# Kernel tuning notes

Measured on AMD Instinct MI355X. Metric: run time of the kernel, lower is better.

The kernel has to match this reference:

```python
import jax, jax.numpy as jnp
import numpy as np

NUM_HEADS = 12


def setup_inputs() -> dict:
    key = jax.random.key(0)
    ks = jax.random.split(key, 5)
    B, N, D = 8, 1024, 768
    x = jax.random.normal(ks[0], (B, N, D), dtype=jnp.float32)
    w_qkv = jax.random.normal(ks[1], (D, 3 * D), dtype=jnp.float32) * (D ** -0.5)
    b_qkv = jax.random.normal(ks[2], (3 * D,), dtype=jnp.float32) * 0.02
    w_proj = jax.random.normal(ks[3], (D, D), dtype=jnp.float32) * (D ** -0.5)
    b_proj = jax.random.normal(ks[4], (D,), dtype=jnp.float32) * 0.02
    return {"x": x, "w_qkv": w_qkv, "b_qkv": b_qkv, "w_proj": w_proj, "b_proj": b_proj}


def reference(x, w_qkv, b_qkv, w_proj, b_proj):
    B, N, D = x.shape
    H = NUM_HEADS
    hd = D // H
    scale = hd ** -0.5
    qkv = x @ w_qkv + b_qkv                      # [B, N, 3D]
    qkv = qkv.reshape(B, N, 3, H, hd)
    q, k, v = jnp.moveaxis(qkv, 2, 0)            # each [B, N, H, hd]
    # scores: [B, H, N, N]
    scores = jnp.einsum("bqhd,bkhd->bhqk", q, k) * scale
    attn = jax.nn.softmax(scores, axis=-1)
    a = jnp.einsum("bhqk,bkhd->bqhd", attn, v)   # [B, N, H, hd]
    a = a.reshape(B, N, D)
    return a @ w_proj + b_proj
```

## Files before the change

kernel.cpp:

```cpp
#include <hip/hip_runtime.h>

#define B_ 8
#define N_ 1024
#define D_ 768
#define H_ 12
#define HD 64
#define M_ (B_*N_)

typedef short short8 __attribute__((ext_vector_type(8)));
typedef float f32x4 __attribute__((ext_vector_type(4)));
typedef float f32x16 __attribute__((ext_vector_type(16)));
typedef int int4v __attribute__((ext_vector_type(4)));

__device__ __forceinline__ unsigned short f2bf(float f) {
    union { float f; unsigned int u; } c; c.f = f;
    unsigned int u = c.u;
    unsigned int r = (u + 0x7fffu + ((u >> 16) & 1u)) >> 16;
    return (unsigned short)r;
}

__device__ __forceinline__ float exp2_hw(float x) {
    float r;
    asm("v_exp_f32 %0, %1" : "=v"(r) : "v"(x));
    return r;
}

__device__ __forceinline__ unsigned int cvtpk_bf16(float a, float b) {
    unsigned int r;
    asm("v_cvt_pk_bf16_f32 %0, %1, %2" : "=v"(r) : "v"(a), "v"(b));
    return r;
}

#define PLSWAP(a, b) asm volatile("v_permlane32_swap_b32 %0, %1" : "+&v"(a), "+&v"(b))

__device__ __forceinline__ short8 pack4(unsigned int a, unsigned int b,
                                        unsigned int c, unsigned int d) {
    union { int4v i; short8 s; } u;
    u.i = (int4v){(int)a, (int)b, (int)c, (int)d};
    return u.s;
}

__device__ __forceinline__ void gload16(const void* g, void* l) {
    __builtin_amdgcn_global_load_lds(
        (const __attribute__((address_space(1))) unsigned int*)g,
        (__attribute__((address_space(3))) unsigned int*)l, 16, 0, 0);
}


__global__ void cast_x_kernel(const float* __restrict__ in,
                              unsigned short* __restrict__ out, int n4) {
    int i = blockIdx.x * blockDim.x + threadIdx.x;
    if (i >= n4) return;
    float4 v = reinterpret_cast<const float4*>(in)[i];
    ushort4 o;
    o.x = f2bf(v.x); o.y = f2bf(v.y); o.z = f2bf(v.z); o.w = f2bf(v.w);
    reinterpret_cast<ushort4*>(out)[i] = o;
}

__global__ void transpose_cast_kernel(const float* __restrict__ w,
                                      unsigned short* __restrict__ wT,
                                      int R, int C) {
    int i = blockIdx.x * blockDim.x + threadIdx.x;
    if (i >= R * C) return;
    int r = i / C, c = i - r * C;
    wT[c * R + r] = f2bf(w[i]);
}

__global__ __launch_bounds__(256) void transpose_v_kernel(
    const unsigned short* __restrict__ vin,
    unsigned short* __restrict__ vout)
{
    __shared__ unsigned short T[64][72];
    int bh = blockIdx.y;
    int n0 = blockIdx.x * 64;
    int t = threadIdx.x;
    int r = t >> 2;
    int c = (t & 3) * 16;
    const uint4* g = reinterpret_cast<const uint4*>(vin + ((size_t)bh * N_ + n0 + r) * HD + c);
    uint4 a = g[0], b2 = g[1];
    *reinterpret_cast<uint4*>(&T[r][c]) = a;
    *reinterpret_cast<uint4*>(&T[r][c + 8]) = b2;
    __syncthreads();
    int d = t >> 2;
    int nc = (t & 3) * 16;
    unsigned short tmp[16];
    #pragma unroll
    for (int j = 0; j < 16; j++) tmp[j] = T[nc + j][d];
    uint4* o = reinterpret_cast<uint4*>(vout + ((size_t)bh * HD + d) * N_ + n0 + nc);
    o[0] = *reinterpret_cast<const uint4*>(&tmp[0]);
    o[1] = *reinterpret_cast<const uint4*>(&tmp[8]);
}


template<int MODE>
__global__ __launch_bounds__(256) void gemm_kernel(
    const unsigned short* __restrict__ A,
    const unsigned short* __restrict__ Bt,
    const float* __restrict__ bias,
    float* __restrict__ outf,
    unsigned short* __restrict__ qo,
    unsigned short* __restrict__ ko,
    unsigned short* __restrict__ vo,
    int Ndim, int K)
{
    __shared__ unsigned short As[128 * 32];
    __shared__ unsigned short Bs[128 * 32];

    int tid = threadIdx.x;
    int lane = tid & 63, w = tid >> 6;
    int wr = w >> 1, wc = w & 1;
    int m0 = blockIdx.y * 128, n0 = blockIdx.x * 128;
    int lr = lane & 15, lk8 = (lane >> 4) * 8;

    int srow = tid >> 2;
    int selem = (tid & 3) * 8;
    const unsigned short* gA = A + (size_t)(m0 + srow) * K + selem;
    const unsigned short* gB = Bt + (size_t)(n0 + srow) * K + selem;
    unsigned short* lA = As + w * 512;
    unsigned short* lB = Bs + w * 512;

    f32x4 acc[4][4] = {};

    for (int k0 = 0; k0 < K; k0 += 32) {
        __syncthreads();
        gload16(gA + k0, lA);
        gload16(gA + (size_t)64 * K + k0, lA + 2048);
        gload16(gB + k0, lB);
        gload16(gB + (size_t)64 * K + k0, lB + 2048);
        __syncthreads();

        short8 af[4], bf[4];
        #pragma unroll
        for (int mi = 0; mi < 4; mi++)
            af[mi] = *reinterpret_cast<const short8*>(&As[(wr * 64 + mi * 16 + lr) * 32 + lk8]);
        #pragma unroll
        for (int ni = 0; ni < 4; ni++)
            bf[ni] = *reinterpret_cast<const short8*>(&Bs[(wc * 64 + ni * 16 + lr) * 32 + lk8]);
        #pragma unroll
        for (int mi = 0; mi < 4; mi++)
            #pragma unroll
            for (int ni = 0; ni < 4; ni++)
                acc[mi][ni] = __builtin_amdgcn_mfma_f32_16x16x32_bf16(af[mi], bf[ni], acc[mi][ni], 0, 0, 0);
    }

    int org = (lane >> 4) * 4;
    if (MODE == 1) {
        #pragma unroll
        for (int mi = 0; mi < 4; mi++) {
            #pragma unroll
            for (int ni = 0; ni < 4; ni++) {
                int col = n0 + wc * 64 + ni * 16 + lr;
                float bv = bias[col];
                #pragma unroll
                for (int r = 0; r < 4; r++) {
                    int row = m0 + wr * 64 + mi * 16 + org + r;
                    outf[(size_t)row * Ndim + col] = acc[mi][ni][r] + bv;
                }
            }
        }
    } else {
        int which = n0 / 768;
        unsigned short* dst = (which == 0) ? qo : (which == 1) ? ko : vo;
        float fold = (which == 0) ? 0.125f * 1.44269504088896f : 1.0f;
        #pragma unroll
        for (int mi = 0; mi < 4; mi++) {
            #pragma unroll
            for (int ni = 0; ni < 4; ni++) {
                int col = n0 + wc * 64 + ni * 16 + lr;
                int rem = col - which * 768;
                int h = rem >> 6, dd = rem & 63;
                float bv = bias[col];
                #pragma unroll
                for (int r = 0; r < 4; r++) {
                    int row = m0 + wr * 64 + mi * 16 + org + r;
                    int b = row >> 10, nn = row & 1023;
                    float o = (acc[mi][ni][r] + bv) * fold;
                    dst[(((size_t)(b * H_ + h) * N_ + nn) * HD) + dd] = f2bf(o);
                }
            }
        }
    }
}


__global__ __launch_bounds__(256) void attn_kernel(
    const unsigned short* __restrict__ qg,
    const unsigned short* __restrict__ kg,
    const unsigned short* __restrict__ vtg,
    unsigned short* __restrict__ aout)
{
    __shared__ alignas(16) unsigned short Ks[2][4096];
    __shared__ alignas(16) unsigned short Vs[2][4096];

    int tid = threadIdx.x;
    int lane = tid & 63, w = tid >> 6;

    int bid = blockIdx.x;
    int xcd = bid & 7;
    int chunk = bid >> 3;
    int bh = xcd * 12 + (chunk % 12);
    int qblk = chunk / 12;
    int b = bh / H_, h = bh - b * H_;
    int q0w = qblk * 128 + w * 32;
    int l31 = lane & 31;
    int hi = lane >> 5;
    int swz = l31 & 7;

    const unsigned short* qp = qg + ((size_t)bh * N_ + q0w + l31) * HD + hi * 8;
    short8 qf[4];
    #pragma unroll
    for (int ds = 0; ds < 4; ds++)
        qf[ds] = *reinterpret_cast<const short8*>(qp + ds * 16);

    const unsigned short* kbh = kg + (size_t)bh * N_ * HD;
    const unsigned short* vtbh = vtg + (size_t)bh * HD * N_;

    int sr0 = tid >> 3;
    int sj0 = (tid & 7) ^ (sr0 & 7);
    int sr1 = sr0 + 32;
    int sj1 = (tid & 7) ^ (sr1 & 7);

    float m_run = -INFINITY, l_run = 0.f;
    f32x16 o0 = {}, o1 = {};

#define STAGE(buf, kv0)                                                        \
    do {                                                                       \
        gload16(kbh + (size_t)((kv0) + sr0) * HD + sj0 * 8, &Ks[buf][w * 512]);\
        gload16(kbh + (size_t)((kv0) + sr1) * HD + sj1 * 8, &Ks[buf][2048 + w * 512]);\
        gload16(vtbh + (size_t)sr0 * N_ + (kv0) + sj0 * 8, &Vs[buf][w * 512]); \
        gload16(vtbh + (size_t)sr1 * N_ + (kv0) + sj1 * 8, &Vs[buf][2048 + w * 512]);\
    } while (0)

    STAGE(0, 0);
    asm volatile("s_waitcnt vmcnt(0)" ::: "memory");
    __builtin_amdgcn_s_barrier();
    __builtin_amdgcn_sched_barrier(0);

    int cur = 0;
    for (int t = 0; t < 16; ++t) {
        if (t < 15) STAGE(cur ^ 1, (t + 1) * 64);

        const unsigned short* Ksb = Ks[cur];
        const unsigned short* Vsb = Vs[cur];

        f32x16 s0 = {}, s1 = {};
        #pragma unroll
        for (int ds = 0; ds < 4; ds++) {
            int pc = (ds * 2 + hi) ^ swz;
            short8 kf0 = *reinterpret_cast<const short8*>(&Ksb[(l31) * 64 + pc * 8]);
            short8 kf1 = *reinterpret_cast<const short8*>(&Ksb[(32 + l31) * 64 + pc * 8]);
            s0 = __builtin_amdgcn_mfma_f32_32x32x16_bf16(kf0, qf[ds], s0, 0, 0, 0);
            s1 = __builtin_amdgcn_mfma_f32_32x32x16_bf16(kf1, qf[ds], s1, 0, 0, 0);
        }

        float mx = s0[0];
        #pragma unroll
        for (int r = 1; r < 16; r++) mx = fmaxf(mx, s0[r]);
        #pragma unroll
        for (int r = 0; r < 16; r++) mx = fmaxf(mx, s1[r]);
        mx = fmaxf(mx, __shfl_xor(mx, 32, 64));

        if (__any(mx > m_run + 8.f)) {
            float mn = fmaxf(m_run, mx);
            float al = exp2_hw(m_run - mn);
            m_run = mn;
            l_run *= al;
            o0 *= al;
            o1 *= al;
        }

        float psum = 0.f;
        #pragma unroll
        for (int r = 0; r < 16; r++) { float p = exp2_hw(s0[r] - m_run); psum += p; s0[r] = p; }
        #pragma unroll
        for (int r = 0; r < 16; r++) { float p = exp2_hw(s1[r] - m_run); psum += p; s1[r] = p; }

        l_run += psum + __shfl_xor(psum, 32, 64);

        unsigned int c0[8], c1[8];
        #pragma unroll
        for (int i = 0; i < 8; i++) c0[i] = cvtpk_bf16(s0[2 * i], s0[2 * i + 1]);
        #pragma unroll
        for (int i = 0; i < 8; i++) c1[i] = cvtpk_bf16(s1[2 * i], s1[2 * i + 1]);
        PLSWAP(c0[0], c0[2]); PLSWAP(c0[1], c0[3]);
        PLSWAP(c0[4], c0[6]); PLSWAP(c0[5], c0[7]);
        PLSWAP(c1[0], c1[2]); PLSWAP(c1[1], c1[3]);
        PLSWAP(c1[4], c1[6]); PLSWAP(c1[5], c1[7]);
        short8 pa0 = pack4(c0[0], c0[1], c0[2], c0[3]);
        short8 pa1 = pack4(c0[4], c0[5], c0[6], c0[7]);
        short8 pa2 = pack4(c1[0], c1[1], c1[2], c1[3]);
        short8 pa3 = pack4(c1[4], c1[5], c1[6], c1[7]);

        #pragma unroll
        for (int ks = 0; ks < 4; ks++) {
            int pc = (ks * 2 + hi) ^ swz;
            short8 vf0 = *reinterpret_cast<const short8*>(&Vsb[(l31) * 64 + pc * 8]);
            short8 vf1 = *reinterpret_cast<const short8*>(&Vsb[(32 + l31) * 64 + pc * 8]);
            short8 pa = (ks == 0) ? pa0 : (ks == 1) ? pa1 : (ks == 2) ? pa2 : pa3;
            o0 = __builtin_amdgcn_mfma_f32_32x32x16_bf16(vf0, pa, o0, 0, 0, 0);
            o1 = __builtin_amdgcn_mfma_f32_32x32x16_bf16(vf1, pa, o1, 0, 0, 0);
        }

        if (t < 15) {
            asm volatile("s_waitcnt vmcnt(0)" ::: "memory");
            __builtin_amdgcn_s_barrier();
            __builtin_amdgcn_sched_barrier(0);
            cur ^= 1;
        }
    }
#undef STAGE

    float linv = 1.0f / l_run;
    unsigned short* op = aout + ((size_t)(b * N_ + q0w + l31)) * D_ + h * HD;
    #pragma unroll
    for (int rg = 0; rg < 4; rg++) {
        int dbase = 8 * rg + 4 * hi;
        unsigned long long u0 = 0, u1 = 0;
        #pragma unroll
        for (int k = 0; k < 4; k++) {
            u0 |= (unsigned long long)f2bf(o0[rg * 4 + k] * linv) << (16 * k);
            u1 |= (unsigned long long)f2bf(o1[rg * 4 + k] * linv) << (16 * k);
        }
        *reinterpret_cast<unsigned long long*>(op + dbase) = u0;
        *reinterpret_cast<unsigned long long*>(op + 32 + dbase) = u1;
    }
}


extern "C" void kernel_launch(void* const* d_in, const int* in_sizes, int n_in,
                              void* d_out, int out_size, void* d_ws, size_t ws_size,
                              hipStream_t stream) {
    const float* x      = (const float*)d_in[0];
    const float* w_qkv  = (const float*)d_in[1];
    const float* b_qkv  = (const float*)d_in[2];
    const float* w_proj = (const float*)d_in[3];
    const float* b_proj = (const float*)d_in[4];
    float* out = (float*)d_out;

    char* ws = (char*)d_ws;
    unsigned short* xb     = (unsigned short*)(ws + 0);
    unsigned short* wqkvT  = (unsigned short*)(ws + 12582912);
    unsigned short* wprojT = (unsigned short*)(ws + 16121856);
    unsigned short* qb     = (unsigned short*)(ws + 17301504);
    unsigned short* kb     = (unsigned short*)(ws + 29884416);
    unsigned short* vb     = (unsigned short*)(ws + 42467328);
    unsigned short* vtb    = (unsigned short*)(ws + 55050240);
    unsigned short* aout   = xb;

    cast_x_kernel<<<6144, 256, 0, stream>>>(x, xb, 1572864);
    transpose_cast_kernel<<<6912, 256, 0, stream>>>(w_qkv, wqkvT, 768, 2304);
    transpose_cast_kernel<<<2304, 256, 0, stream>>>(w_proj, wprojT, 768, 768);

    gemm_kernel<0><<<dim3(18, 64), 256, 0, stream>>>(
        xb, wqkvT, b_qkv, nullptr, qb, kb, vb, 3 * D_, D_);

    transpose_v_kernel<<<dim3(16, 96), 256, 0, stream>>>(vb, vtb);

    attn_kernel<<<768, 256, 0, stream>>>(qb, kb, vtb, aout);

    gemm_kernel<1><<<dim3(6, 64), 256, 0, stream>>>(
        aout, wprojT, b_proj, out, nullptr, nullptr, nullptr, D_, D_);
}
```

Measured before the change: 148.3 us.

## Merge prep kernels, double-buffer GEMM, fuse V transpose into QKV epilogue

Merges the three cast/transpose kernels into one launch. Double-buffers the GEMM's LDS tiles so the next k-slice loads while the current one is multiplied, and remaps the 1D grid so consecutive blocks are spread across XCDs. V is written already transposed from the QKV GEMM epilogue, which removes the separate transpose kernel and its round trip through memory. Q/K outputs are staged through LDS so each thread writes 16-byte vectors instead of scattered 2-byte stores. This adds code complexity and uses more LDS per GEMM block, which may lower occupancy.

```diff
diff --git a/kernel.cpp b/kernel.cpp
--- a/kernel.cpp
+++ b/kernel.cpp
@@ -47,48 +47,28 @@
 }
 
 
-__global__ void cast_x_kernel(const float* __restrict__ in,
-                              unsigned short* __restrict__ out, int n4) {
-    int i = blockIdx.x * blockDim.x + threadIdx.x;
-    if (i >= n4) return;
-    float4 v = reinterpret_cast<const float4*>(in)[i];
-    ushort4 o;
-    o.x = f2bf(v.x); o.y = f2bf(v.y); o.z = f2bf(v.z); o.w = f2bf(v.w);
-    reinterpret_cast<ushort4*>(out)[i] = o;
-}
-
-__global__ void transpose_cast_kernel(const float* __restrict__ w,
-                                      unsigned short* __restrict__ wT,
-                                      int R, int C) {
-    int i = blockIdx.x * blockDim.x + threadIdx.x;
-    if (i >= R * C) return;
-    int r = i / C, c = i - r * C;
-    wT[c * R + r] = f2bf(w[i]);
-}
-
-__global__ __launch_bounds__(256) void transpose_v_kernel(
-    const unsigned short* __restrict__ vin,
-    unsigned short* __restrict__ vout)
+__global__ __launch_bounds__(256) void prep_kernel(
+    const float* __restrict__ x, const float* __restrict__ wqkv,
+    const float* __restrict__ wproj,
+    unsigned short* __restrict__ xb, unsigned short* __restrict__ wqkvT,
+    unsigned short* __restrict__ wprojT)
 {
-    __shared__ unsigned short T[64][72];
-    int bh = blockIdx.y;
-    int n0 = blockIdx.x * 64;
-    int t = threadIdx.x;
-    int r = t >> 2;
-    int c = (t & 3) * 16;
-    const uint4* g = reinterpret_cast<const uint4*>(vin + ((size_t)bh * N_ + n0 + r) * HD + c);
-    uint4 a = g[0], b2 = g[1];
-    *reinterpret_cast<uint4*>(&T[r][c]) = a;
-    *reinterpret_cast<uint4*>(&T[r][c + 8]) = b2;
-    __syncthreads();
-    int d = t >> 2;
-    int nc = (t & 3) * 16;
-    unsigned short tmp[16];
-    #pragma unroll
-    for (int j = 0; j < 16; j++) tmp[j] = T[nc + j][d];
-    uint4* o = reinterpret_cast<uint4*>(vout + ((size_t)bh * HD + d) * N_ + n0 + nc);
-    o[0] = *reinterpret_cast<const uint4*>(&tmp[0]);
-    o[1] = *reinterpret_cast<const uint4*>(&tmp[8]);
+    int bid = blockIdx.x, tid = threadIdx.x;
+    if (bid < 6144) {
+        int i = bid * 256 + tid;
+        float4 v = reinterpret_cast<const float4*>(x)[i];
+        ushort4 o;
+        o.x = f2bf(v.x); o.y = f2bf(v.y); o.z = f2bf(v.z); o.w = f2bf(v.w);
+        reinterpret_cast<ushort4*>(xb)[i] = o;
+    } else if (bid < 6144 + 6912) {
+        int i = (bid - 6144) * 256 + tid;
+        int r = i / 2304, c = i - r * 2304;
+        wqkvT[c * 768 + r] = f2bf(wqkv[i]);
+    } else {
+        int i = (bid - 13056) * 256 + tid;
+        int r = i / 768, c = i - r * 768;
+        wprojT[c * 768 + r] = f2bf(wproj[i]);
+    }
 }
 
 
@@ -103,47 +83,73 @@
     unsigned short* __restrict__ vo,
     int Ndim, int K)
 {
-    __shared__ unsigned short As[128 * 32];
-    __shared__ unsigned short Bs[128 * 32];
+    __shared__ alignas(16) unsigned short smem[16384];
+    unsigned short* As0 = smem;
+    unsigned short* Bs0 = smem + 8192;
 
     int tid = threadIdx.x;
     int lane = tid & 63, w = tid >> 6;
     int wr = w >> 1, wc = w & 1;
-    int m0 = blockIdx.y * 128, n0 = blockIdx.x * 128;
+
+    int nbx = Ndim >> 7;
+    int nwg = gridDim.x;
+    int cpx = nwg >> 3;
+    int sbid = (blockIdx.x & 7) * cpx + (blockIdx.x >> 3);
+    int bx = sbid % nbx, by = sbid / nbx;
+    int m0 = by * 128, n0 = bx * 128;
+
     int lr = lane & 15, lk8 = (lane >> 4) * 8;
+    int org = (lane >> 4) * 4;
 
     int srow = tid >> 2;
     int selem = (tid & 3) * 8;
     const unsigned short* gA = A + (size_t)(m0 + srow) * K + selem;
     const unsigned short* gB = Bt + (size_t)(n0 + srow) * K + selem;
-    unsigned short* lA = As + w * 512;
-    unsigned short* lB = Bs + w * 512;
 
     f32x4 acc[4][4] = {};
 
-    for (int k0 = 0; k0 < K; k0 += 32) {
-        __syncthreads();
-        gload16(gA + k0, lA);
-        gload16(gA + (size_t)64 * K + k0, lA + 2048);
-        gload16(gB + k0, lB);
-        gload16(gB + (size_t)64 * K + k0, lB + 2048);
-        __syncthreads();
-
+#define GSTAGE(buf, k0)                                                    \
+    do {                                                                   \
+        gload16(gA + (k0), As0 + (buf) * 4096 + w * 512);                  \
+        gload16(gA + (size_t)64 * K + (k0), As0 + (buf) * 4096 + 2048 + w * 512);\
+        gload16(gB + (k0), Bs0 + (buf) * 4096 + w * 512);                  \
+        gload16(gB + (size_t)64 * K + (k0), Bs0 + (buf) * 4096 + 2048 + w * 512);\
+    } while (0)
+
+    GSTAGE(0, 0);
+    asm volatile("s_waitcnt vmcnt(0)" ::: "memory");
+    __builtin_amdgcn_s_barrier();
+    __builtin_amdgcn_sched_barrier(0);
+
+    int KT = K >> 5;
+    int cur = 0;
+    for (int kt = 0; kt < KT; ++kt) {
+        if (kt + 1 < KT) GSTAGE(cur ^ 1, (kt + 1) * 32);
+
+        const unsigned short* Ab = As0 + cur * 4096;
+        const unsigned short* Bb = Bs0 + cur * 4096;
         short8 af[4], bf[4];
         #pragma unroll
         for (int mi = 0; mi < 4; mi++)
-            af[mi] = *reinterpret_cast<const short8*>(&As[(wr * 64 + mi * 16 + lr) * 32 + lk8]);
+            af[mi] = *reinterpret_cast<const short8*>(&Ab[(wr * 64 + mi * 16 + lr) * 32 + lk8]);
         #pragma unroll
         for (int ni = 0; ni < 4; ni++)
-            bf[ni] = *reinterpret_cast<const short8*>(&Bs[(wc * 64 + ni * 16 + lr) * 32 + lk8]);
+            bf[ni] = *reinterpret_cast<const short8*>(&Bb[(wc * 64 + ni * 16 + lr) * 32 + lk8]);
         #pragma unroll
         for (int mi = 0; mi < 4; mi++)
             #pragma unroll
             for (int ni = 0; ni < 4; ni++)
                 acc[mi][ni] = __builtin_amdgcn_mfma_f32_16x16x32_bf16(af[mi], bf[ni], acc[mi][ni], 0, 0, 0);
-    }
-
-    int org = (lane >> 4) * 4;
+
+        if (kt + 1 < KT) {
+            asm volatile("s_waitcnt vmcnt(0)" ::: "memory");
+            __builtin_amdgcn_s_barrier();
+            __builtin_amdgcn_sched_barrier(0);
+            cur ^= 1;
+        }
+    }
+#undef GSTAGE
+
     if (MODE == 1) {
         #pragma unroll
         for (int mi = 0; mi < 4; mi++) {
@@ -158,26 +164,59 @@
                 }
             }
         }
-    } else {
-        int which = n0 / 768;
-        unsigned short* dst = (which == 0) ? qo : (which == 1) ? ko : vo;
-        float fold = (which == 0) ? 0.125f * 1.44269504088896f : 1.0f;
+        return;
+    }
+
+    int which = n0 / 768;
+    if (which == 2) {
         #pragma unroll
         for (int mi = 0; mi < 4; mi++) {
+            int nn0g = m0 + wr * 64 + mi * 16 + org;
+            int b = nn0g >> 10, nn = nn0g & 1023;
             #pragma unroll
             for (int ni = 0; ni < 4; ni++) {
-                int col = n0 + wc * 64 + ni * 16 + lr;
-                int rem = col - which * 768;
+                int colg = n0 + wc * 64 + ni * 16 + lr;
+                int rem = colg - 1536;
                 int h = rem >> 6, dd = rem & 63;
-                float bv = bias[col];
+                float bv = bias[colg];
+                unsigned long long u = 0;
                 #pragma unroll
-                for (int r = 0; r < 4; r++) {
-                    int row = m0 + wr * 64 + mi * 16 + org + r;
-                    int b = row >> 10, nn = row & 1023;
-                    float o = (acc[mi][ni][r] + bv) * fold;
-                    dst[(((size_t)(b * H_ + h) * N_ + nn) * HD) + dd] = f2bf(o);
+                for (int r = 0; r < 4; r++)
+                    u |= (unsigned long long)f2bf(acc[mi][ni][r] + bv) << (16 * r);
+                *reinterpret_cast<unsigned long long*>(
+                    vo + ((size_t)(b * H_ + h) * HD + dd) * N_ + nn) = u;
+            }
+        }
+    } else {
+        unsigned short* dst = (which == 0) ? qo : ko;
+        float fold = (which == 0) ? 0.125f * 1.44269504088896f : 1.0f;
+        unsigned short* T = smem;
+        __syncthreads();
+        #pragma unroll
+        for (int hc = 0; hc < 2; ++hc) {
+            if (hc) __syncthreads();
+            if (wc == hc) {
+                #pragma unroll
+                for (int mi = 0; mi < 4; mi++) {
+                    int rl = wr * 64 + mi * 16 + org;
+                    #pragma unroll
+                    for (int ni = 0; ni < 4; ni++) {
+                        int cl = ni * 16 + lr;
+                        float bv = bias[n0 + hc * 64 + cl];
+                        #pragma unroll
+                        for (int r = 0; r < 4; r++)
+                            T[(rl + r) * 72 + cl] = f2bf((acc[mi][ni][r] + bv) * fold);
+                    }
                 }
             }
+            __syncthreads();
+            int row = tid >> 1, c0 = (tid & 1) * 32;
+            int h = (n0 + hc * 64 - which * 768) >> 6;
+            int nng = m0 + row;
+            int b = nng >> 10, nn = nng & 1023;
+            const uint4* src = reinterpret_cast<const uint4*>(&T[row * 72 + c0]);
+            uint4* dv = reinterpret_cast<uint4*>(dst + ((size_t)(b * H_ + h) * N_ + nn) * HD + c0);
+            dv[0] = src[0]; dv[1] = src[1]; dv[2] = src[2]; dv[3] = src[3];
         }
     }
 }
@@ -343,21 +382,16 @@
     unsigned short* wprojT = (unsigned short*)(ws + 16121856);
     unsigned short* qb     = (unsigned short*)(ws + 17301504);
     unsigned short* kb     = (unsigned short*)(ws + 29884416);
-    unsigned short* vb     = (unsigned short*)(ws + 42467328);
-    unsigned short* vtb    = (unsigned short*)(ws + 55050240);
+    unsigned short* vtb    = (unsigned short*)(ws + 42467328);
     unsigned short* aout   = xb;
 
-    cast_x_kernel<<<6144, 256, 0, stream>>>(x, xb, 1572864);
-    transpose_cast_kernel<<<6912, 256, 0, stream>>>(w_qkv, wqkvT, 768, 2304);
-    transpose_cast_kernel<<<2304, 256, 0, stream>>>(w_proj, wprojT, 768, 768);
-
-    gemm_kernel<0><<<dim3(18, 64), 256, 0, stream>>>(
-        xb, wqkvT, b_qkv, nullptr, qb, kb, vb, 3 * D_, D_);
-
-    transpose_v_kernel<<<dim3(16, 96), 256, 0, stream>>>(vb, vtb);
+    prep_kernel<<<15360, 256, 0, stream>>>(x, w_qkv, w_proj, xb, wqkvT, wprojT);
+
+    gemm_kernel<0><<<1152, 256, 0, stream>>>(
+        xb, wqkvT, b_qkv, nullptr, qb, kb, vtb, 3 * D_, D_);
 
     attn_kernel<<<768, 256, 0, stream>>>(qb, kb, vtb, aout);
 
-    gemm_kernel<1><<<dim3(6, 64), 256, 0, stream>>>(
+    gemm_kernel<1><<<384, 256, 0, stream>>>(
         aout, wprojT, b_proj, out, nullptr, nullptr, nullptr, D_, D_);
 }
```

After: 136.2 us. -8.2%, faster.
